# Kernel optimization log

Hardware: AMD Instinct MI355X
Metric: run time of the kernel (lower is better)

The kernel has to match this reference:

```python
import jax, jax.numpy as jnp
import numpy as np

DIM = 256
NUM_HEADS = 8
HEAD_DIM = DIM // NUM_HEADS


def setup_inputs() -> dict:
    key = jax.random.key(0)
    k1, k2, k3, k4 = jax.random.split(key, 4)
    b, n = 4, 2048
    x = jax.random.normal(k1, (b, n, DIM), dtype=jnp.float32)
    # Linear weights with fan-in scaling (matches nn.Linear init magnitude,
    # keeps exp(qk) numerically sane since the original has no max-subtraction).
    Wqkv = jax.random.normal(k2, (DIM, 3 * DIM), dtype=jnp.float32) * (DIM ** -0.5)
    Wout = jax.random.normal(k3, (DIM, DIM), dtype=jnp.float32) * (DIM ** -0.5)
    bout = jax.random.normal(k4, (DIM,), dtype=jnp.float32) * 0.01
    return {"x": x, "Wqkv": Wqkv, "Wout": Wout, "bout": bout}


def reference(x, Wqkv, Wout, bout):
    b, n, d = x.shape
    h, hd = NUM_HEADS, HEAD_DIM
    scale = hd ** -0.5
    qkv = x @ Wqkv  # [b, n, 3d]
    q, k, v = jnp.split(qkv, 3, axis=-1)
    # [b, h, n, hd]
    q = q.reshape(b, n, h, hd).transpose(0, 2, 1, 3) * scale
    k = k.reshape(b, n, h, hd).transpose(0, 2, 1, 3)
    v = v.reshape(b, n, h, hd).transpose(0, 2, 1, 3)
    # Original KeOps path: unnormalized exp (no max-subtraction), separate
    # numerator / denominator reductions, eps in denominator.
    scores = jnp.einsum('bhnd,bhmd->bhnm', q, k)  # [b, h, n, n]
    e = jnp.exp(scores)
    denom = jnp.sum(e, axis=-1, keepdims=True)          # [b, h, n, 1]
    numer = jnp.einsum('bhnm,bhmd->bhnd', e, v)         # [b, h, n, hd]
    out = numer / (denom + 1e-6)
    out = out.transpose(0, 2, 1, 3).reshape(b, n, d)
    return out @ Wout + bout
```

## Files before the change

kernel.cpp:

```cpp
#include <hip/hip_runtime.h>

#define DIM 256
#define NHEADS 8
#define HDIM 32

typedef _Float16 half8_t __attribute__((ext_vector_type(8)));
typedef _Float16 half4_t __attribute__((ext_vector_type(4)));
typedef float float4_t __attribute__((ext_vector_type(4)));

__device__ __forceinline__ float fast_exp2(float x) {
#if __has_builtin(__builtin_amdgcn_exp2f)
    return __builtin_amdgcn_exp2f(x);
#else
    return __expf(x * 0.6931471805599453f);
#endif
}

__device__ __forceinline__ void gload_lds16(const void* g, void* l) {
    __builtin_amdgcn_global_load_lds((const __attribute__((address_space(1))) void*)g,
                                     (__attribute__((address_space(3))) void*)l,
                                     16, 0, 0);
}

__global__ __launch_bounds__(256) void prep(const float* __restrict__ x,
                                            const float* __restrict__ Wqkv,
                                            const float* __restrict__ Wout,
                                            _Float16* __restrict__ xh,
                                            _Float16* __restrict__ WqT,
                                            _Float16* __restrict__ WoT) {
    __shared__ float ts[32][33];
    const int bid = blockIdx.x, t = threadIdx.x;
    if (bid < 1024) {
        size_t idx = (size_t)bid * 2048 + (size_t)t * 8;
        float tmp[8];
        *reinterpret_cast<float4*>(tmp)     = *reinterpret_cast<const float4*>(x + idx);
        *reinterpret_cast<float4*>(tmp + 4) = *reinterpret_cast<const float4*>(x + idx + 4);
        half8_t h;
        #pragma unroll
        for (int j = 0; j < 8; ++j) h[j] = (_Float16)tmp[j];
        *reinterpret_cast<half8_t*>(xh + idx) = h;
    } else {
        const float* src; _Float16* dst; int K, N, kb, nb;
        if (bid < 1024 + 192) { int b2 = bid - 1024; src = Wqkv; dst = WqT; K = 256; N = 768; nb = b2 % 24; kb = b2 / 24; }
        else                  { int b3 = bid - 1216; src = Wout; dst = WoT; K = 256; N = 256; nb = b3 % 8;  kb = b3 / 8; }
        const int tx = t & 31, ty = t >> 5;
        #pragma unroll
        for (int i = 0; i < 4; ++i) {
            int k = kb * 32 + ty + i * 8;
            ts[ty + i * 8][tx] = src[(size_t)k * N + nb * 32 + tx];
        }
        __syncthreads();
        #pragma unroll
        for (int i = 0; i < 4; ++i) {
            int nl = ty + i * 8;
            dst[(size_t)(nb * 32 + nl) * K + kb * 32 + tx] = (_Float16)ts[tx][nl];
        }
    }
}

template <bool OUT_HALF, bool VSPLIT, int MROWS>
__global__ __launch_bounds__(256) void gemm_h(const _Float16* __restrict__ A,
                                              const _Float16* __restrict__ BT,
                                              const float* __restrict__ bias,
                                              void* __restrict__ Cv,
                                              _Float16* __restrict__ VTo,
                                              int M, int N, int K, int ldc) {
    constexpr int BM = MROWS * 32;
    __shared__ alignas(16) _Float16 As[BM * 32];
    __shared__ alignas(16) _Float16 Bs[128 * 32];
    const int t = threadIdx.x, lane = t & 63, wave = t >> 6;
    const int l16 = lane & 15, quad = lane >> 4;
    const int m0 = blockIdx.y * BM, n0 = blockIdx.x * 128;
    const int wr = (wave >> 1) * (MROWS * 16), wc = (wave & 1) * 64;
    constexpr float QS = 0.17677669529663687f * 1.4426950408889634f;
    float4_t acc[MROWS][4];
    #pragma unroll
    for (int i = 0; i < MROWS; ++i)
        #pragma unroll
        for (int j = 0; j < 4; ++j) acc[i][j] = (float4_t){0.f, 0.f, 0.f, 0.f};

    const int srow = lane >> 2;
    const int scol = (lane & 3) * 8;

    for (int k0 = 0; k0 < K; k0 += 32) {
        #pragma unroll
        for (int i = 0; i < MROWS / 2; ++i) {
            int chunk = i * 4 + wave;
            int r = chunk * 16 + srow;
            gload_lds16(A + (size_t)(m0 + r) * K + k0 + scol, As + chunk * 512);
        }
        #pragma unroll
        for (int i = 0; i < 2; ++i) {
            int chunk = i * 4 + wave;
            int r = chunk * 16 + srow;
            gload_lds16(BT + (size_t)(n0 + r) * K + k0 + scol, Bs + chunk * 512);
        }
        __syncthreads();
        half8_t af[MROWS], bf[4];
        #pragma unroll
        for (int i = 0; i < MROWS; ++i)
            af[i] = *reinterpret_cast<const half8_t*>(As + (wr + i * 16 + l16) * 32 + quad * 8);
        #pragma unroll
        for (int j = 0; j < 4; ++j)
            bf[j] = *reinterpret_cast<const half8_t*>(Bs + (wc + j * 16 + l16) * 32 + quad * 8);
        #pragma unroll
        for (int i = 0; i < MROWS; ++i)
            #pragma unroll
            for (int j = 0; j < 4; ++j)
                acc[i][j] = __builtin_amdgcn_mfma_f32_16x16x32_f16(af[i], bf[j], acc[i][j], 0, 0, 0);
        __syncthreads();
    }

    if (VSPLIT && n0 >= 512) {
        const int bb = m0 >> 11;
        const int tok0 = (m0 & 2047) + wr;
        #pragma unroll
        for (int i = 0; i < MROWS; ++i)
            #pragma unroll
            for (int j = 0; j < 4; ++j) {
                int vcol = n0 + wc + j * 16 + l16 - 512;
                int hh = vcol >> 5, d = vcol & 31;
                half4_t p;
                #pragma unroll
                for (int r = 0; r < 4; ++r) p[r] = (_Float16)acc[i][j][r];
                *reinterpret_cast<half4_t*>(
                    VTo + ((size_t)(bb * NHEADS + hh) * HDIM + d) * 2048
                        + tok0 + i * 16 + quad * 4) = p;
            }
    } else {
        float bv[4] = {0.f, 0.f, 0.f, 0.f};
        if (bias != nullptr) {
            #pragma unroll
            for (int j = 0; j < 4; ++j) bv[j] = bias[n0 + wc + j * 16 + l16];
        }
        #pragma unroll
        for (int i = 0; i < MROWS; ++i)
            #pragma unroll
            for (int r = 0; r < 4; ++r) {
                int row = m0 + wr + i * 16 + quad * 4 + r;
                #pragma unroll
                for (int j = 0; j < 4; ++j) {
                    int col = n0 + wc + j * 16 + l16;
                    float v = acc[i][j][r] + bv[j];
                    if (VSPLIT && n0 < 256) v *= QS;
                    if (OUT_HALF) ((_Float16*)Cv)[(size_t)row * ldc + col] = (_Float16)v;
                    else          ((float*)Cv)[(size_t)row * ldc + col] = v;
                }
            }
    }
}

__global__ __launch_bounds__(256, 2) void attn_v7(const _Float16* __restrict__ qkh,
                                                  const _Float16* __restrict__ VT,
                                                  _Float16* __restrict__ NUM,
                                                  float* __restrict__ DEN) {
    __shared__ alignas(16) _Float16 es[4][64][40];
    const int bid = blockIdx.x;
    const int kh = bid & 1;
    const int qb = (bid >> 1) & 7;
    const int bh = bid >> 4;
    const int b = bh >> 3, h = bh & 7;
    const int t = threadIdx.x, lane = t & 63, wave = t >> 6;
    const int l16 = lane & 15, quad = lane >> 4;
    const int bN = b * 2048;
    const int q0w = qb * 256 + wave * 64;
    const int kbeg = kh * 1024;

    half8_t qf[4];
    {
        const _Float16* qrow = qkh + (size_t)(bN + q0w + l16) * 512 + h * HDIM + quad * 8;
        #pragma unroll
        for (int g = 0; g < 4; ++g)
            qf[g] = *reinterpret_cast<const half8_t*>(qrow + (size_t)g * 16 * 512);
    }

    const _Float16* kbase = qkh + (size_t)(bN + l16) * 512 + 256 + h * HDIM + quad * 8;
    const _Float16* vbase = VT + (size_t)bh * HDIM * 2048 + (size_t)l16 * 2048 + quad * 8;

    float4_t num[4][2];
    #pragma unroll
    for (int g = 0; g < 4; ++g)
        #pragma unroll
        for (int dt = 0; dt < 2; ++dt) num[g][dt] = (float4_t){0.f, 0.f, 0.f, 0.f};
    float4_t dacc[4];
    #pragma unroll
    for (int g = 0; g < 4; ++g) dacc[g] = (float4_t){0.f, 0.f, 0.f, 0.f};

    half8_t onef;
    #pragma unroll
    for (int j = 0; j < 8; ++j) onef[j] = (_Float16)1.0f;

    _Float16* esw = &es[wave][0][0];
    const float4_t z = {0.f, 0.f, 0.f, 0.f};

    for (int k0 = kbeg; k0 < kbeg + 1024; k0 += 64) {
        const _Float16* kp = kbase + (size_t)k0 * 512;
        half8_t kf[4], vf[4];
        #pragma unroll
        for (int j = 0; j < 4; ++j)
            kf[j] = *reinterpret_cast<const half8_t*>(kp + (size_t)j * 16 * 512);
        const _Float16* vp = vbase + k0;
        vf[0] = *reinterpret_cast<const half8_t*>(vp);
        vf[1] = *reinterpret_cast<const half8_t*>(vp + (size_t)16 * 2048);
        vf[2] = *reinterpret_cast<const half8_t*>(vp + 32);
        vf[3] = *reinterpret_cast<const half8_t*>(vp + 32 + (size_t)16 * 2048);

        half4_t ep[4][4];
        #pragma unroll
        for (int kb = 0; kb < 4; ++kb)
            #pragma unroll
            for (int g = 0; g < 4; ++g) {
                float4_t st = __builtin_amdgcn_mfma_f32_16x16x32_f16(kf[kb], qf[g], z, 0, 0, 0);
                auto lo = __builtin_amdgcn_cvt_pkrtz(fast_exp2(st[0]), fast_exp2(st[1]));
                auto hi = __builtin_amdgcn_cvt_pkrtz(fast_exp2(st[2]), fast_exp2(st[3]));
                ep[kb][g] = (half4_t){(_Float16)lo[0], (_Float16)lo[1],
                                      (_Float16)hi[0], (_Float16)hi[1]};
            }

        #pragma unroll
        for (int s = 0; s < 2; ++s) {
            #pragma unroll
            for (int tt = 0; tt < 2; ++tt)
                #pragma unroll
                for (int g = 0; g < 4; ++g)
                    *reinterpret_cast<half4_t*>(
                        esw + (g * 16 + l16) * 40 + tt * 16 + quad * 4) = ep[s * 2 + tt][g];

            #pragma unroll
            for (int g = 0; g < 4; ++g) {
                half8_t ef = *reinterpret_cast<const half8_t*>(
                    esw + (g * 16 + l16) * 40 + quad * 8);
                num[g][0] = __builtin_amdgcn_mfma_f32_16x16x32_f16(ef, vf[s * 2],     num[g][0], 0, 0, 0);
                num[g][1] = __builtin_amdgcn_mfma_f32_16x16x32_f16(ef, vf[s * 2 + 1], num[g][1], 0, 0, 0);
                dacc[g]   = __builtin_amdgcn_mfma_f32_16x16x32_f16(ef, onef,          dacc[g],   0, 0, 0);
            }
        }
    }

    _Float16* ob = NUM + (size_t)kh * 2097152 + (size_t)(bN + q0w) * DIM + h * HDIM;
    #pragma unroll
    for (int g = 0; g < 4; ++g)
        #pragma unroll
        for (int r = 0; r < 4; ++r) {
            size_t ro = (size_t)(g * 16 + quad * 4 + r) * DIM;
            ob[ro + l16]      = (_Float16)num[g][0][r];
            ob[ro + 16 + l16] = (_Float16)num[g][1][r];
        }
    if (l16 == 0) {
        #pragma unroll
        for (int g = 0; g < 4; ++g)
            #pragma unroll
            for (int r = 0; r < 4; ++r)
                DEN[kh * 65536 + bh * 2048 + q0w + g * 16 + quad * 4 + r] = dacc[g][r];
    }
}

__global__ __launch_bounds__(256) void combine(const _Float16* __restrict__ NUM,
                                               const float* __restrict__ DEN,
                                               _Float16* __restrict__ attnh) {
    const size_t idx = ((size_t)blockIdx.x * 256 + threadIdx.x) * 8;
    const int row = (int)(idx >> 8);
    const int c = (int)(idx & 255);
    const int b = row >> 11, tok = row & 2047, h = c >> 5;
    const int di = (b * 8 + h) * 2048 + tok;
    float rcp = 1.0f / (DEN[di] + DEN[di + 65536] + 1e-6f);
    half8_t n0 = *reinterpret_cast<const half8_t*>(NUM + idx);
    half8_t n1 = *reinterpret_cast<const half8_t*>(NUM + idx + 2097152);
    *reinterpret_cast<half8_t*>(attnh + idx) = (n0 + n1) * (_Float16)rcp;
}

extern "C" void kernel_launch(void* const* d_in, const int* in_sizes, int n_in,
                              void* d_out, int out_size, void* d_ws, size_t ws_size,
                              hipStream_t stream) {
    const float* x    = (const float*)d_in[0];
    const float* Wqkv = (const float*)d_in[1];
    const float* Wout = (const float*)d_in[2];
    const float* bout = (const float*)d_in[3];
    float* out = (float*)d_out;
    const int M = 8192;

    _Float16* xh    = (_Float16*)d_ws;
    _Float16* WqT   = xh + (size_t)M * DIM;
    _Float16* WoT   = WqT + 768 * 256;
    _Float16* qkh   = WoT + 256 * 256;
    _Float16* vt    = qkh + (size_t)M * 512;
    _Float16* NUM   = vt + (size_t)32 * HDIM * 2048;
    float*    DEN   = (float*)(NUM + (size_t)2 * M * DIM);
    _Float16* attnh = (_Float16*)(DEN + 2 * 65536);

    hipLaunchKernelGGL(prep, dim3(1280), dim3(256), 0, stream, x, Wqkv, Wout, xh, WqT, WoT);
    hipLaunchKernelGGL((gemm_h<true, true, 4>), dim3(6, 64), dim3(256), 0, stream,
                       xh, WqT, (const float*)nullptr, (void*)qkh, vt, M, 768, DIM, 512);
    hipLaunchKernelGGL(attn_v7, dim3(512), dim3(256), 0, stream, qkh, vt, NUM, DEN);
    hipLaunchKernelGGL(combine, dim3(1024), dim3(256), 0, stream, NUM, DEN, attnh);
    hipLaunchKernelGGL((gemm_h<false, false, 2>), dim3(2, 128), dim3(256), 0, stream,
                       attnh, WoT, bout, (void*)out, (_Float16*)nullptr, M, DIM, DIM, DIM);
}
```

Baseline: 127.2 us.

## Drop split-K attention, fuse normalization, double-buffer K/V register loads

The attention kernel no longer splits the key range in two halves. Each block now covers 128 queries (32 per wave) over all 2048 keys and normalizes in-kernel, which removes the combine kernel and the NUM/DEN workspace traffic. K/V fragments are double-buffered in registers (A/B sets) so the next tile's loads overlap the current tile's MFMA and exp work. Each wave now holds fewer queries, so every K/V load is reused across fewer rows and more total K/V bandwidth is spent per query.

```diff
diff --git a/kernel.cpp b/kernel.cpp
--- a/kernel.cpp
+++ b/kernel.cpp
@@ -150,41 +150,88 @@
     }
 }
 
-__global__ __launch_bounds__(256, 2) void attn_v7(const _Float16* __restrict__ qkh,
+
+#define LOADKV(P, k0)                                                              \
+    do {                                                                           \
+        const _Float16* kp_ = kbase + (size_t)(k0) * 512;                          \
+        k##P##0 = *reinterpret_cast<const half8_t*>(kp_);                          \
+        k##P##1 = *reinterpret_cast<const half8_t*>(kp_ + (size_t)16 * 512);       \
+        k##P##2 = *reinterpret_cast<const half8_t*>(kp_ + (size_t)32 * 512);       \
+        k##P##3 = *reinterpret_cast<const half8_t*>(kp_ + (size_t)48 * 512);       \
+        const _Float16* vp_ = vbase + (k0);                                        \
+        v##P##0 = *reinterpret_cast<const half8_t*>(vp_);                          \
+        v##P##1 = *reinterpret_cast<const half8_t*>(vp_ + (size_t)16 * 2048);      \
+        v##P##2 = *reinterpret_cast<const half8_t*>(vp_ + 32);                     \
+        v##P##3 = *reinterpret_cast<const half8_t*>(vp_ + 32 + (size_t)16 * 2048); \
+    } while (0)
+
+#define EXPKB(KF, e0, e1)                                                          \
+    do {                                                                           \
+        float4_t st0 = __builtin_amdgcn_mfma_f32_16x16x32_f16(KF, qf0, z, 0, 0, 0);\
+        float4_t st1 = __builtin_amdgcn_mfma_f32_16x16x32_f16(KF, qf1, z, 0, 0, 0);\
+        auto lo0 = __builtin_amdgcn_cvt_pkrtz(fast_exp2(st0[0]), fast_exp2(st0[1]));\
+        auto hi0 = __builtin_amdgcn_cvt_pkrtz(fast_exp2(st0[2]), fast_exp2(st0[3]));\
+        e0 = (half4_t){(_Float16)lo0[0], (_Float16)lo0[1],                         \
+                       (_Float16)hi0[0], (_Float16)hi0[1]};                        \
+        auto lo1 = __builtin_amdgcn_cvt_pkrtz(fast_exp2(st1[0]), fast_exp2(st1[1]));\
+        auto hi1 = __builtin_amdgcn_cvt_pkrtz(fast_exp2(st1[2]), fast_exp2(st1[3]));\
+        e1 = (half4_t){(_Float16)lo1[0], (_Float16)lo1[1],                         \
+                       (_Float16)hi1[0], (_Float16)hi1[1]};                        \
+    } while (0)
+
+#define PVCHUNK(ea0, ea1, eb0, eb1, VF0, VF1)                                      \
+    do {                                                                           \
+        *reinterpret_cast<half4_t*>(esw + l16 * 40 + quad * 4) = ea0;              \
+        *reinterpret_cast<half4_t*>(esw + (16 + l16) * 40 + quad * 4) = ea1;       \
+        *reinterpret_cast<half4_t*>(esw + l16 * 40 + 16 + quad * 4) = eb0;         \
+        *reinterpret_cast<half4_t*>(esw + (16 + l16) * 40 + 16 + quad * 4) = eb1;  \
+        half8_t ef0 = *reinterpret_cast<const half8_t*>(esw + l16 * 40 + quad * 8);\
+        half8_t ef1 = *reinterpret_cast<const half8_t*>(esw + (16 + l16) * 40 + quad * 8);\
+        num00 = __builtin_amdgcn_mfma_f32_16x16x32_f16(ef0, VF0, num00, 0, 0, 0);  \
+        num01 = __builtin_amdgcn_mfma_f32_16x16x32_f16(ef0, VF1, num01, 0, 0, 0);  \
+        dacc0 = __builtin_amdgcn_mfma_f32_16x16x32_f16(ef0, onef, dacc0, 0, 0, 0); \
+        num10 = __builtin_amdgcn_mfma_f32_16x16x32_f16(ef1, VF0, num10, 0, 0, 0);  \
+        num11 = __builtin_amdgcn_mfma_f32_16x16x32_f16(ef1, VF1, num11, 0, 0, 0);  \
+        dacc1 = __builtin_amdgcn_mfma_f32_16x16x32_f16(ef1, onef, dacc1, 0, 0, 0); \
+    } while (0)
+
+#define STEP(P)                                                                    \
+    do {                                                                           \
+        half4_t e00, e01, e10, e11, e20, e21, e30, e31;                            \
+        EXPKB(k##P##0, e00, e01);                                                  \
+        EXPKB(k##P##1, e10, e11);                                                  \
+        EXPKB(k##P##2, e20, e21);                                                  \
+        EXPKB(k##P##3, e30, e31);                                                  \
+        PVCHUNK(e00, e01, e10, e11, v##P##0, v##P##1);                             \
+        PVCHUNK(e20, e21, e30, e31, v##P##2, v##P##3);                             \
+    } while (0)
+
+__global__ __launch_bounds__(256, 2) void attn_v8(const _Float16* __restrict__ qkh,
                                                   const _Float16* __restrict__ VT,
-                                                  _Float16* __restrict__ NUM,
-                                                  float* __restrict__ DEN) {
-    __shared__ alignas(16) _Float16 es[4][64][40];
+                                                  _Float16* __restrict__ attnh) {
+    __shared__ alignas(16) _Float16 es[4][32][40];
     const int bid = blockIdx.x;
-    const int kh = bid & 1;
-    const int qb = (bid >> 1) & 7;
+    const int qb = bid & 15;
     const int bh = bid >> 4;
     const int b = bh >> 3, h = bh & 7;
     const int t = threadIdx.x, lane = t & 63, wave = t >> 6;
     const int l16 = lane & 15, quad = lane >> 4;
     const int bN = b * 2048;
-    const int q0w = qb * 256 + wave * 64;
-    const int kbeg = kh * 1024;
-
-    half8_t qf[4];
+    const int q0w = qb * 128 + wave * 32;
+
+    half8_t qf0, qf1;
     {
         const _Float16* qrow = qkh + (size_t)(bN + q0w + l16) * 512 + h * HDIM + quad * 8;
-        #pragma unroll
-        for (int g = 0; g < 4; ++g)
-            qf[g] = *reinterpret_cast<const half8_t*>(qrow + (size_t)g * 16 * 512);
+        qf0 = *reinterpret_cast<const half8_t*>(qrow);
+        qf1 = *reinterpret_cast<const half8_t*>(qrow + (size_t)16 * 512);
     }
 
     const _Float16* kbase = qkh + (size_t)(bN + l16) * 512 + 256 + h * HDIM + quad * 8;
     const _Float16* vbase = VT + (size_t)bh * HDIM * 2048 + (size_t)l16 * 2048 + quad * 8;
 
-    float4_t num[4][2];
-    #pragma unroll
-    for (int g = 0; g < 4; ++g)
-        #pragma unroll
-        for (int dt = 0; dt < 2; ++dt) num[g][dt] = (float4_t){0.f, 0.f, 0.f, 0.f};
-    float4_t dacc[4];
-    #pragma unroll
-    for (int g = 0; g < 4; ++g) dacc[g] = (float4_t){0.f, 0.f, 0.f, 0.f};
+    float4_t num00 = {0.f, 0.f, 0.f, 0.f}, num01 = {0.f, 0.f, 0.f, 0.f};
+    float4_t num10 = {0.f, 0.f, 0.f, 0.f}, num11 = {0.f, 0.f, 0.f, 0.f};
+    float4_t dacc0 = {0.f, 0.f, 0.f, 0.f}, dacc1 = {0.f, 0.f, 0.f, 0.f};
 
     half8_t onef;
     #pragma unroll
@@ -193,80 +240,29 @@
     _Float16* esw = &es[wave][0][0];
     const float4_t z = {0.f, 0.f, 0.f, 0.f};
 
-    for (int k0 = kbeg; k0 < kbeg + 1024; k0 += 64) {
-        const _Float16* kp = kbase + (size_t)k0 * 512;
-        half8_t kf[4], vf[4];
-        #pragma unroll
-        for (int j = 0; j < 4; ++j)
-            kf[j] = *reinterpret_cast<const half8_t*>(kp + (size_t)j * 16 * 512);
-        const _Float16* vp = vbase + k0;
-        vf[0] = *reinterpret_cast<const half8_t*>(vp);
-        vf[1] = *reinterpret_cast<const half8_t*>(vp + (size_t)16 * 2048);
-        vf[2] = *reinterpret_cast<const half8_t*>(vp + 32);
-        vf[3] = *reinterpret_cast<const half8_t*>(vp + 32 + (size_t)16 * 2048);
-
-        half4_t ep[4][4];
-        #pragma unroll
-        for (int kb = 0; kb < 4; ++kb)
-            #pragma unroll
-            for (int g = 0; g < 4; ++g) {
-                float4_t st = __builtin_amdgcn_mfma_f32_16x16x32_f16(kf[kb], qf[g], z, 0, 0, 0);
-                auto lo = __builtin_amdgcn_cvt_pkrtz(fast_exp2(st[0]), fast_exp2(st[1]));
-                auto hi = __builtin_amdgcn_cvt_pkrtz(fast_exp2(st[2]), fast_exp2(st[3]));
-                ep[kb][g] = (half4_t){(_Float16)lo[0], (_Float16)lo[1],
-                                      (_Float16)hi[0], (_Float16)hi[1]};
-            }
-
-        #pragma unroll
-        for (int s = 0; s < 2; ++s) {
-            #pragma unroll
-            for (int tt = 0; tt < 2; ++tt)
-                #pragma unroll
-                for (int g = 0; g < 4; ++g)
-                    *reinterpret_cast<half4_t*>(
-                        esw + (g * 16 + l16) * 40 + tt * 16 + quad * 4) = ep[s * 2 + tt][g];
-
-            #pragma unroll
-            for (int g = 0; g < 4; ++g) {
-                half8_t ef = *reinterpret_cast<const half8_t*>(
-                    esw + (g * 16 + l16) * 40 + quad * 8);
-                num[g][0] = __builtin_amdgcn_mfma_f32_16x16x32_f16(ef, vf[s * 2],     num[g][0], 0, 0, 0);
-                num[g][1] = __builtin_amdgcn_mfma_f32_16x16x32_f16(ef, vf[s * 2 + 1], num[g][1], 0, 0, 0);
-                dacc[g]   = __builtin_amdgcn_mfma_f32_16x16x32_f16(ef, onef,          dacc[g],   0, 0, 0);
-            }
-        }
-    }
-
-    _Float16* ob = NUM + (size_t)kh * 2097152 + (size_t)(bN + q0w) * DIM + h * HDIM;
+    half8_t kA0, kA1, kA2, kA3, vA0, vA1, vA2, vA3;
+    half8_t kB0, kB1, kB2, kB3, vB0, vB1, vB2, vB3;
+    LOADKV(A, 0);
+    #pragma unroll 2
+    for (int k0 = 0; k0 < 2048; k0 += 128) {
+        LOADKV(B, k0 + 64);
+        STEP(A);
+        if (k0 + 128 < 2048) LOADKV(A, k0 + 128);
+        STEP(B);
+    }
+
+    _Float16* ob = attnh + (size_t)(bN + q0w) * DIM + h * HDIM;
     #pragma unroll
-    for (int g = 0; g < 4; ++g)
-        #pragma unroll
-        for (int r = 0; r < 4; ++r) {
-            size_t ro = (size_t)(g * 16 + quad * 4 + r) * DIM;
-            ob[ro + l16]      = (_Float16)num[g][0][r];
-            ob[ro + 16 + l16] = (_Float16)num[g][1][r];
-        }
-    if (l16 == 0) {
-        #pragma unroll
-        for (int g = 0; g < 4; ++g)
-            #pragma unroll
-            for (int r = 0; r < 4; ++r)
-                DEN[kh * 65536 + bh * 2048 + q0w + g * 16 + quad * 4 + r] = dacc[g][r];
-    }
-}
-
-__global__ __launch_bounds__(256) void combine(const _Float16* __restrict__ NUM,
-                                               const float* __restrict__ DEN,
-                                               _Float16* __restrict__ attnh) {
-    const size_t idx = ((size_t)blockIdx.x * 256 + threadIdx.x) * 8;
-    const int row = (int)(idx >> 8);
-    const int c = (int)(idx & 255);
-    const int b = row >> 11, tok = row & 2047, h = c >> 5;
-    const int di = (b * 8 + h) * 2048 + tok;
-    float rcp = 1.0f / (DEN[di] + DEN[di + 65536] + 1e-6f);
-    half8_t n0 = *reinterpret_cast<const half8_t*>(NUM + idx);
-    half8_t n1 = *reinterpret_cast<const half8_t*>(NUM + idx + 2097152);
-    *reinterpret_cast<half8_t*>(attnh + idx) = (n0 + n1) * (_Float16)rcp;
+    for (int r = 0; r < 4; ++r) {
+        float rcp0 = 1.0f / (dacc0[r] + 1e-6f);
+        float rcp1 = 1.0f / (dacc1[r] + 1e-6f);
+        size_t ro0 = (size_t)(quad * 4 + r) * DIM;
+        size_t ro1 = (size_t)(16 + quad * 4 + r) * DIM;
+        ob[ro0 + l16]      = (_Float16)(num00[r] * rcp0);
+        ob[ro0 + 16 + l16] = (_Float16)(num01[r] * rcp0);
+        ob[ro1 + l16]      = (_Float16)(num10[r] * rcp1);
+        ob[ro1 + 16 + l16] = (_Float16)(num11[r] * rcp1);
+    }
 }
 
 extern "C" void kernel_launch(void* const* d_in, const int* in_sizes, int n_in,
@@ -284,15 +280,12 @@
     _Float16* WoT   = WqT + 768 * 256;
     _Float16* qkh   = WoT + 256 * 256;
     _Float16* vt    = qkh + (size_t)M * 512;
-    _Float16* NUM   = vt + (size_t)32 * HDIM * 2048;
-    float*    DEN   = (float*)(NUM + (size_t)2 * M * DIM);
-    _Float16* attnh = (_Float16*)(DEN + 2 * 65536);
+    _Float16* attnh = vt + (size_t)32 * HDIM * 2048;
 
     hipLaunchKernelGGL(prep, dim3(1280), dim3(256), 0, stream, x, Wqkv, Wout, xh, WqT, WoT);
     hipLaunchKernelGGL((gemm_h<true, true, 4>), dim3(6, 64), dim3(256), 0, stream,
                        xh, WqT, (const float*)nullptr, (void*)qkh, vt, M, 768, DIM, 512);
-    hipLaunchKernelGGL(attn_v7, dim3(512), dim3(256), 0, stream, qkh, vt, NUM, DEN);
-    hipLaunchKernelGGL(combine, dim3(1024), dim3(256), 0, stream, NUM, DEN, attnh);
+    hipLaunchKernelGGL(attn_v8, dim3(512), dim3(256), 0, stream, qkh, vt, attnh);
     hipLaunchKernelGGL((gemm_h<false, false, 2>), dim3(2, 128), dim3(256), 0, stream,
                        attnh, WoT, bout, (void*)out, (_Float16*)nullptr, M, DIM, DIM, DIM);
 }
```

New measurement: 146.2 us. 15.0% more time.

## Double-buffer K/V loads with inline asm, remap blocks, shrink QKV GEMM tile

Applied to the files above, without the earlier changes.

Rewrites the attention main loop to double-buffer K and V fragments. It issues the next tile's global loads through inline asm and uses explicit vmcnt waits and sched barriers, so memory latency overlaps with the MFMA and exp work. It also swizzles the block index so neighbouring blocks map to different (b,h) groups, and halves the M tile of the QKV projection GEMM to launch more blocks. The risks are higher register pressure, and the hand-written waits rely on the compiler not reordering around them.

```diff
diff --git a/kernel.cpp b/kernel.cpp
--- a/kernel.cpp
+++ b/kernel.cpp
@@ -150,12 +150,71 @@
     }
 }
 
-__global__ __launch_bounds__(256, 2) void attn_v7(const _Float16* __restrict__ qkh,
-                                                  const _Float16* __restrict__ VT,
-                                                  _Float16* __restrict__ NUM,
-                                                  float* __restrict__ DEN) {
+
+#define GLD(dst, addr) \
+    asm volatile("global_load_dwordx4 %0, %1, off" : "=v"(dst) : "v"(addr))
+#define WAITV(N) asm volatile("s_waitcnt vmcnt(" #N ")" ::: "memory")
+#define SB0 __builtin_amdgcn_sched_barrier(0)
+
+#define LOADASM(P, k0)                                            \
+    do {                                                          \
+        const _Float16* kp_ = kbase + (size_t)(k0) * 512;         \
+        GLD(k##P[0], kp_);                                        \
+        GLD(k##P[1], kp_ + (size_t)16 * 512);                     \
+        GLD(k##P[2], kp_ + (size_t)32 * 512);                     \
+        GLD(k##P[3], kp_ + (size_t)48 * 512);                     \
+        const _Float16* vp_ = vbase + (k0);                       \
+        GLD(v##P[0], vp_);                                        \
+        GLD(v##P[1], vp_ + (size_t)16 * 2048);                    \
+        GLD(v##P[2], vp_ + 32);                                   \
+        GLD(v##P[3], vp_ + 32 + (size_t)16 * 2048);               \
+    } while (0)
+
+#define STEP(P)                                                                    \
+    do {                                                                           \
+        half4_t ep[4][4];                                                          \
+        _Pragma("unroll")                                                          \
+        for (int kb = 0; kb < 4; ++kb)                                             \
+            _Pragma("unroll")                                                      \
+            for (int g = 0; g < 4; ++g) {                                          \
+                float4_t st = __builtin_amdgcn_mfma_f32_16x16x32_f16(              \
+                    k##P[kb], qf[g], z, 0, 0, 0);                                  \
+                auto lo = __builtin_amdgcn_cvt_pkrtz(fast_exp2(st[0]),             \
+                                                     fast_exp2(st[1]));            \
+                auto hi = __builtin_amdgcn_cvt_pkrtz(fast_exp2(st[2]),             \
+                                                     fast_exp2(st[3]));            \
+                ep[kb][g] = (half4_t){(_Float16)lo[0], (_Float16)lo[1],            \
+                                      (_Float16)hi[0], (_Float16)hi[1]};           \
+            }                                                                      \
+        _Pragma("unroll")                                                          \
+        for (int s = 0; s < 2; ++s) {                                              \
+            _Pragma("unroll")                                                      \
+            for (int tt = 0; tt < 2; ++tt)                                         \
+                _Pragma("unroll")                                                  \
+                for (int g = 0; g < 4; ++g)                                        \
+                    *reinterpret_cast<half4_t*>(                                   \
+                        esw + (g * 16 + l16) * 40 + tt * 16 + quad * 4) =          \
+                        ep[s * 2 + tt][g];                                         \
+            _Pragma("unroll")                                                      \
+            for (int g = 0; g < 4; ++g) {                                          \
+                half8_t ef = *reinterpret_cast<const half8_t*>(                    \
+                    esw + (g * 16 + l16) * 40 + quad * 8);                         \
+                num[g][0] = __builtin_amdgcn_mfma_f32_16x16x32_f16(                \
+                    ef, v##P[s * 2], num[g][0], 0, 0, 0);                          \
+                num[g][1] = __builtin_amdgcn_mfma_f32_16x16x32_f16(                \
+                    ef, v##P[s * 2 + 1], num[g][1], 0, 0, 0);                      \
+                dacc[g] = __builtin_amdgcn_mfma_f32_16x16x32_f16(                  \
+                    ef, onef, dacc[g], 0, 0, 0);                                   \
+            }                                                                      \
+        }                                                                          \
+    } while (0)
+
+__global__ __launch_bounds__(256, 2) void attn_v11(const _Float16* __restrict__ qkh,
+                                                   const _Float16* __restrict__ VT,
+                                                   _Float16* __restrict__ NUM,
+                                                   float* __restrict__ DEN) {
     __shared__ alignas(16) _Float16 es[4][64][40];
-    const int bid = blockIdx.x;
+    const int bid = ((blockIdx.x & 7) << 6) | (blockIdx.x >> 3);
     const int kh = bid & 1;
     const int qb = (bid >> 1) & 7;
     const int bh = bid >> 4;
@@ -166,75 +225,49 @@
     const int q0w = qb * 256 + wave * 64;
     const int kbeg = kh * 1024;
 
+    const _Float16* kbase = qkh + (size_t)(bN + l16) * 512 + 256 + h * HDIM + quad * 8;
+    const _Float16* vbase = VT + (size_t)bh * HDIM * 2048 + (size_t)l16 * 2048 + quad * 8;
+
+    float4_t num[4][2];
+    #pragma unroll
+    for (int g = 0; g < 4; ++g)
+        #pragma unroll
+        for (int dt = 0; dt < 2; ++dt) num[g][dt] = (float4_t){0.f, 0.f, 0.f, 0.f};
+    float4_t dacc[4];
+    #pragma unroll
+    for (int g = 0; g < 4; ++g) dacc[g] = (float4_t){0.f, 0.f, 0.f, 0.f};
+
+    half8_t onef;
+    #pragma unroll
+    for (int j = 0; j < 8; ++j) onef[j] = (_Float16)1.0f;
+
+    _Float16* esw = &es[wave][0][0];
+    const float4_t z = {0.f, 0.f, 0.f, 0.f};
+
     half8_t qf[4];
     {
         const _Float16* qrow = qkh + (size_t)(bN + q0w + l16) * 512 + h * HDIM + quad * 8;
-        #pragma unroll
-        for (int g = 0; g < 4; ++g)
-            qf[g] = *reinterpret_cast<const half8_t*>(qrow + (size_t)g * 16 * 512);
-    }
-
-    const _Float16* kbase = qkh + (size_t)(bN + l16) * 512 + 256 + h * HDIM + quad * 8;
-    const _Float16* vbase = VT + (size_t)bh * HDIM * 2048 + (size_t)l16 * 2048 + quad * 8;
-
-    float4_t num[4][2];
-    #pragma unroll
-    for (int g = 0; g < 4; ++g)
-        #pragma unroll
-        for (int dt = 0; dt < 2; ++dt) num[g][dt] = (float4_t){0.f, 0.f, 0.f, 0.f};
-    float4_t dacc[4];
-    #pragma unroll
-    for (int g = 0; g < 4; ++g) dacc[g] = (float4_t){0.f, 0.f, 0.f, 0.f};
-
-    half8_t onef;
-    #pragma unroll
-    for (int j = 0; j < 8; ++j) onef[j] = (_Float16)1.0f;
-
-    _Float16* esw = &es[wave][0][0];
-    const float4_t z = {0.f, 0.f, 0.f, 0.f};
-
-    for (int k0 = kbeg; k0 < kbeg + 1024; k0 += 64) {
-        const _Float16* kp = kbase + (size_t)k0 * 512;
-        half8_t kf[4], vf[4];
-        #pragma unroll
-        for (int j = 0; j < 4; ++j)
-            kf[j] = *reinterpret_cast<const half8_t*>(kp + (size_t)j * 16 * 512);
-        const _Float16* vp = vbase + k0;
-        vf[0] = *reinterpret_cast<const half8_t*>(vp);
-        vf[1] = *reinterpret_cast<const half8_t*>(vp + (size_t)16 * 2048);
-        vf[2] = *reinterpret_cast<const half8_t*>(vp + 32);
-        vf[3] = *reinterpret_cast<const half8_t*>(vp + 32 + (size_t)16 * 2048);
-
-        half4_t ep[4][4];
-        #pragma unroll
-        for (int kb = 0; kb < 4; ++kb)
-            #pragma unroll
-            for (int g = 0; g < 4; ++g) {
-                float4_t st = __builtin_amdgcn_mfma_f32_16x16x32_f16(kf[kb], qf[g], z, 0, 0, 0);
-                auto lo = __builtin_amdgcn_cvt_pkrtz(fast_exp2(st[0]), fast_exp2(st[1]));
-                auto hi = __builtin_amdgcn_cvt_pkrtz(fast_exp2(st[2]), fast_exp2(st[3]));
-                ep[kb][g] = (half4_t){(_Float16)lo[0], (_Float16)lo[1],
-                                      (_Float16)hi[0], (_Float16)hi[1]};
-            }
-
-        #pragma unroll
-        for (int s = 0; s < 2; ++s) {
-            #pragma unroll
-            for (int tt = 0; tt < 2; ++tt)
-                #pragma unroll
-                for (int g = 0; g < 4; ++g)
-                    *reinterpret_cast<half4_t*>(
-                        esw + (g * 16 + l16) * 40 + tt * 16 + quad * 4) = ep[s * 2 + tt][g];
-
-            #pragma unroll
-            for (int g = 0; g < 4; ++g) {
-                half8_t ef = *reinterpret_cast<const half8_t*>(
-                    esw + (g * 16 + l16) * 40 + quad * 8);
-                num[g][0] = __builtin_amdgcn_mfma_f32_16x16x32_f16(ef, vf[s * 2],     num[g][0], 0, 0, 0);
-                num[g][1] = __builtin_amdgcn_mfma_f32_16x16x32_f16(ef, vf[s * 2 + 1], num[g][1], 0, 0, 0);
-                dacc[g]   = __builtin_amdgcn_mfma_f32_16x16x32_f16(ef, onef,          dacc[g],   0, 0, 0);
-            }
-        }
+        GLD(qf[0], qrow);
+        GLD(qf[1], qrow + (size_t)16 * 512);
+        GLD(qf[2], qrow + (size_t)32 * 512);
+        GLD(qf[3], qrow + (size_t)48 * 512);
+    }
+
+    half8_t kA[4], vA[4], kB[4], vB[4];
+    LOADASM(A, kbeg);
+    for (int k0 = kbeg; k0 < kbeg + 1024; k0 += 128) {
+        LOADASM(B, k0 + 64);
+        WAITV(8);
+        SB0;
+        STEP(A);
+        if (k0 + 128 < kbeg + 1024) {
+            LOADASM(A, k0 + 128);
+            WAITV(8);
+        } else {
+            WAITV(0);
+        }
+        SB0;
+        STEP(B);
     }
 
     _Float16* ob = NUM + (size_t)kh * 2097152 + (size_t)(bN + q0w) * DIM + h * HDIM;
@@ -289,9 +322,9 @@
     _Float16* attnh = (_Float16*)(DEN + 2 * 65536);
 
     hipLaunchKernelGGL(prep, dim3(1280), dim3(256), 0, stream, x, Wqkv, Wout, xh, WqT, WoT);
-    hipLaunchKernelGGL((gemm_h<true, true, 4>), dim3(6, 64), dim3(256), 0, stream,
+    hipLaunchKernelGGL((gemm_h<true, true, 2>), dim3(6, 128), dim3(256), 0, stream,
                        xh, WqT, (const float*)nullptr, (void*)qkh, vt, M, 768, DIM, 512);
-    hipLaunchKernelGGL(attn_v7, dim3(512), dim3(256), 0, stream, qkh, vt, NUM, DEN);
+    hipLaunchKernelGGL(attn_v11, dim3(512), dim3(256), 0, stream, qkh, vt, NUM, DEN);
     hipLaunchKernelGGL(combine, dim3(1024), dim3(256), 0, stream, NUM, DEN, attnh);
     hipLaunchKernelGGL((gemm_h<false, false, 2>), dim3(2, 128), dim3(256), 0, stream,
                        attnh, WoT, bout, (void*)out, (_Float16*)nullptr, M, DIM, DIM, DIM);
```

After: 120.8 us. -5.0%, faster.
